# Performance work log

Measured on AMD Instinct MI355X. Metric: run time of the kernel, lower is better.

## Reference

```python
import jax, jax.numpy as jnp
import numpy as np
import math
from jax import lax

NUM_POS = 128        # random_choice in pos_neg_sampling
NUM_TOT = 256        # pos + (128 + negative_padding) always totals 256
POS_W = 10.0         # positive_weight in compute_loss


def _conv(x, w, b, pad):
    y = lax.conv_general_dilated(x, w, (1, 1), pad,
                                 dimension_numbers=('NCHW', 'OIHW', 'NCHW'))
    return y + b[None, :, None, None]


def make_anchor_box(img_h, img_w, gh, gw):
    # torch.range(0, W, W/(gw-1)) == inclusive linspace with gw points
    xs = jnp.linspace(0.0, float(img_w), gw)
    ys = jnp.linspace(0.0, float(img_h), gh)
    gx, gy = jnp.meshgrid(xs, ys, indexing='ij')          # (gw, gh) like torch.meshgrid
    xy = jnp.stack([gx.reshape(-1), gy.reshape(-1)], -1).reshape(gh, gw, 2)
    whs = []
    for area in (128 * 128, 256 * 256, 512 * 512):
        for wr, hr in ((1, 1), (2, 1), (1, 2)):
            u = math.sqrt(area / (wr * hr))
            whs.append((wr * u, hr * u))
    wh = jnp.asarray(whs, jnp.float32)                    # (9, 2)
    xy9 = jnp.broadcast_to(xy[:, :, None, :], (gh, gw, 9, 2))
    wh9 = jnp.broadcast_to(wh[None, None], (gh, gw, 9, 2))
    boxes = jnp.concatenate([xy9, xy9 + wh9], -1)         # x1,y1,x2,y2
    return boxes.reshape(-1, 4)


def pairwise_iou(t, a):
    # t: [T,4], a: [A,4], xyxy -> [T,A]
    lt = jnp.maximum(t[:, None, :2], a[None, :, :2])
    rb = jnp.minimum(t[:, None, 2:], a[None, :, 2:])
    wh = jnp.clip(rb - lt, 0.0)
    inter = wh[..., 0] * wh[..., 1]
    at = (t[:, 2] - t[:, 0]) * (t[:, 3] - t[:, 1])
    aa = (a[:, 2] - a[:, 0]) * (a[:, 3] - a[:, 1])
    return inter / (at[:, None] + aa[None, :] - inter)


def box_encode(anchor, bbox):
    awh = anchor[:, 2:] - anchor[:, :2]
    bwh = bbox[:, 2:] - bbox[:, :2]
    ac = anchor[:, :2] + awh / 2
    bc = bbox[:, :2] + bwh / 2
    dxy = (bc - ac) / awh
    dwh = jnp.log(bwh / awh)
    return jnp.concatenate([dxy, dwh], 1)


def rpn_forward(x, target, conv_w, conv_b, bbox_w, bbox_b, score_w, score_b,
                img_h, img_w):
    gh, gw = x.shape[-2], x.shape[-1]
    h = jax.nn.relu(_conv(x[None], conv_w, conv_b, 'SAME'))
    bbox = jax.nn.relu(_conv(h, bbox_w, bbox_b, 'VALID')).reshape(-1, 4)   # [A,4]
    score = jax.nn.relu(_conv(h, score_w, score_b, 'VALID')).reshape(-1, 2)  # [A,2]
    anchors = make_anchor_box(img_h, img_w, gh, gw)                        # [A,4]

    iou = pairwise_iou(target, anchors)                                    # [T,A]
    max_iou = iou.max(0)
    tgt_idx = jnp.argmax(iou, 0)

    # deterministic replacement for np.random.choice sampling (fixed shapes)
    pos_score = jnp.where(max_iou > 0.7, max_iou, -1.0)
    pos_vals, pos_idx = lax.top_k(pos_score, NUM_POS)
    pos_valid = pos_vals > 0.0
    n_pos = jnp.sum(pos_valid.astype(jnp.int32))

    neg_score = jnp.where(max_iou < 0.3, 1.0 - max_iou, -1.0)
    neg_vals, neg_idx = lax.top_k(neg_score, NUM_TOT)
    neg_valid = (neg_vals > 0.0) & (jnp.arange(NUM_TOT) < (NUM_TOT - n_pos))

    bbox_pred = bbox[pos_idx]                                              # [128,4]
    scores_sel = score[jnp.concatenate([pos_idx, neg_idx])]                # [384,2]
    valid = jnp.concatenate([pos_valid, neg_valid]).astype(jnp.float32)

    tgt_scores = jnp.concatenate([
        jnp.tile(jnp.asarray([[1.0, 0.0]], jnp.float32), (NUM_POS, 1)),
        jnp.tile(jnp.asarray([[0.0, 1.0]], jnp.float32), (NUM_TOT, 1))], 0)

    matched = target[tgt_idx[pos_idx]]
    treg = box_encode(anchors[pos_idx], matched)

    ce = -jnp.sum(tgt_scores * jax.nn.log_softmax(scores_sel, -1), -1)
    score_loss = jnp.sum(ce * valid) / jnp.maximum(jnp.sum(valid), 1.0)

    d = bbox_pred - treg
    sl1 = jnp.where(jnp.abs(d) < 1.0, 0.5 * d * d, jnp.abs(d) - 0.5)
    pm = pos_valid.astype(jnp.float32)[:, None]
    reg_loss = jnp.sum(sl1 * pm) / jnp.maximum(jnp.sum(pm) * 4.0, 1.0)

    return score_loss + POS_W * reg_loss


def setup_inputs():
    key = jax.random.key(0)
    ks = jax.random.split(key, 8)
    cin, gh, gw, nt = 512, 128, 128, 64
    x = jax.random.normal(ks[0], (cin, gh, gw), jnp.float32)
    cxy = jax.random.uniform(ks[1], (nt, 2), minval=300.0, maxval=1748.0)
    wh = jax.random.uniform(ks[2], (nt, 2), minval=64.0, maxval=512.0)
    target = jnp.concatenate([cxy - wh / 2, cxy + wh / 2], -1)
    conv_w = jax.random.normal(ks[3], (cin, cin, 3, 3), jnp.float32) * 0.02
    conv_b = jnp.zeros((cin,), jnp.float32)
    bbox_w = jax.random.normal(ks[4], (36, cin, 1, 1), jnp.float32) * 0.02
    bbox_b = jnp.zeros((36,), jnp.float32)
    score_w = jax.random.normal(ks[5], (18, cin, 1, 1), jnp.float32) * 0.02
    score_b = jnp.zeros((18,), jnp.float32)
    return {'x': x, 'target': target, 'conv_w': conv_w, 'conv_b': conv_b,
            'bbox_w': bbox_w, 'bbox_b': bbox_b, 'score_w': score_w,
            'score_b': score_b, 'img_h': 2048, 'img_w': 2048}


def reference(x, target, conv_w, conv_b, bbox_w, bbox_b, score_w, score_b,
              img_h, img_w):
    return rpn_forward(x, target, conv_w, conv_b, bbox_w, bbox_b,
                       score_w, score_b, img_h, img_w)
```

## Files before the change

kernel.cpp:

```cpp
#include <hip/hip_runtime.h>
#include <cstdint>
#include <cstddef>

typedef unsigned long long ull;
typedef __bf16 bf16x8 __attribute__((ext_vector_type(8)));
typedef float f32x4 __attribute__((ext_vector_type(4)));

#define NA     147456
#define NT     64
#define KDIM   4608
#define NTASK  1280
#define CAND_CAP 4096
#define KSPLIT 4
#define NIOUB  576
#define NTRB   2048
#define NPREP2 512
#define NIMCB  2880

#define OFF_WB2   0
#define OFF_P2    4718592
#define OFF_H4    16515072
#define OFF_XT    27000832
#define OFF_MIOU  43778048
#define OFF_CAND  44367872
#define OFF_CPB   45547520
#define OFF_CBZ   45549824
#define OFF_NPOS  45552128
#define OFF_POSA  45552132
#define OFF_TREG  45552648
#define OFF_TASKS 45554696
#define OFF_OUT   45559816

#define UANC 90.509667991878f
__device__ __constant__ float WKa[9] = {128.0f, 2.0f*UANC, UANC, 256.0f, 4.0f*UANC, 2.0f*UANC, 512.0f, 8.0f*UANC, 4.0f*UANC};
__device__ __constant__ float HKa[9] = {128.0f, UANC, 2.0f*UANC, 256.0f, 2.0f*UANC, 4.0f*UANC, 512.0f, 4.0f*UANC, 8.0f*UANC};

__device__ __forceinline__ float iou_one(float x1, float y1, float x2, float y2, float4 t) {
#pragma clang fp contract(off)
  float ltx = fmaxf(t.x, x1), lty = fmaxf(t.y, y1);
  float rbx = fminf(t.z, x2), rby = fminf(t.w, y2);
  float wx = fmaxf(rbx - ltx, 0.0f);
  float wy = fmaxf(rby - lty, 0.0f);
  float inter = wx * wy;
  float at = (t.z - t.x) * (t.w - t.y);
  float aa = (x2 - x1) * (y2 - y1);
  return inter / ((at + aa) - inter);
}

__device__ __forceinline__ unsigned short f2bf(float f) {
  unsigned int u = __float_as_uint(f);
  unsigned int r = (u + 0x7fffu + ((u >> 16) & 1u)) >> 16;
  return (unsigned short)r;
}

__global__ __launch_bounds__(256) void k_pi(const float* __restrict__ cw,
    unsigned short* __restrict__ Wb2, const float* __restrict__ x,
    unsigned short* __restrict__ xtb,
    const float* __restrict__ tgt, const int* __restrict__ imw,
    const int* __restrict__ imh, float* __restrict__ miou,
    ull* __restrict__ cand, int* __restrict__ cpb, int* __restrict__ cbz) {
  __shared__ __align__(16) char smem[20480];
  int blk = blockIdx.x;
  int tid = threadIdx.x;
  if (blk >= NIOUB + NTRB) {
    float* row = (float*)smem;
    int m = blk - (NIOUB + NTRB);
    const float* src = cw + (size_t)m * KDIM;
    for (int f = tid; f < KDIM; f += 256) {
      int cin = f / 9;
      row[cin * 10 + (f - cin * 9)] = src[f];
    }
    __syncthreads();
    for (int kc = tid; kc < 576; kc += 256) {
      int r = kc >> 6, c8 = kc & 63;
      int base = c8 * 80 + r;
      unsigned short o[8];
      #pragma unroll
      for (int j = 0; j < 8; ++j) o[j] = f2bf(row[base + j * 10]);
      *(uint4*)(Wb2 + ((size_t)kc * 512 + m) * 8) = *(const uint4*)o;
    }
    return;
  }
  if (blk >= NIOUB) {
    float* tile = (float*)smem;
    int tb = blk - NIOUB;
    int pix0 = (tb & 255) * 64;
    int cin0 = (tb >> 8) * 64;
    int pr = tid & 15, cr = tid >> 4;
    #pragma unroll
    for (int i = 0; i < 4; ++i) {
      int cin = cr + i * 16;
      float4 v = *(const float4*)(x + (size_t)(cin0 + cin) * 16384 + pix0 + pr * 4);
      tile[cin * 65 + pr * 4 + 0] = v.x;
      tile[cin * 65 + pr * 4 + 1] = v.y;
      tile[cin * 65 + pr * 4 + 2] = v.z;
      tile[cin * 65 + pr * 4 + 3] = v.w;
    }
    __syncthreads();
    #pragma unroll
    for (int i = 0; i < 4; ++i) {
      int pix = cr + i * 16;
      unsigned short o[4] = {f2bf(tile[(pr * 4 + 0) * 65 + pix]),
                             f2bf(tile[(pr * 4 + 1) * 65 + pix]),
                             f2bf(tile[(pr * 4 + 2) * 65 + pix]),
                             f2bf(tile[(pr * 4 + 3) * 65 + pix])};
      *(uint2*)(xtb + (size_t)(pix0 + pix) * 512 + cin0 + pr * 4) = *(const uint2*)o;
    }
    return;
  }
  float4* ts = (float4*)smem;
  int* wz = (int*)(smem + 1024);
  int* wc = wz + 4;
  if (tid < NT) ts[tid] = ((const float4*)tgt)[tid];
  __syncthreads();
  int a = blk * 256 + tid;
  int k = a % 9;
  int pq = a / 9;
  int p = pq >> 7, q = pq & 127;
  float dx = (float)(*imw) / 127.0f;
  float dyl = (float)(*imh) / 127.0f;
  float x1 = (float)p * dx, y1 = (float)q * dyl;
  float x2 = x1 + WKa[k], y2 = y1 + HKa[k];
  float best = -1.0f;
  #pragma unroll 8
  for (int t = 0; t < NT; ++t) best = fmaxf(best, iou_one(x1, y1, x2, y2, ts[t]));
  miou[a] = best;
  int lane = tid & 63, w = tid >> 6;
  ull bz = __ballot(best == 0.0f);
  bool isc = best > 0.7f;
  ull bc = __ballot(isc);
  if (lane == 0) { wz[w] = (int)__popcll(bz); wc[w] = (int)__popcll(bc); }
  __syncthreads();
  if (tid == 0) {
    cbz[blk] = wz[0] + wz[1] + wz[2] + wz[3];
    cpb[blk] = wc[0] + wc[1] + wc[2] + wc[3];
  }
  if (isc) {
    int woff = 0;
    for (int i = 0; i < w; ++i) woff += wc[i];
    int rank = woff + (int)__popcll(bc & ((1ull << lane) - 1ull));
    cand[blk * 256 + rank] = ((ull)__float_as_uint(best) << 32) | (ull)(0xFFFFFFFFu - (unsigned)a);
  }
}

__global__ __launch_bounds__(256) void k_selA(const ull* __restrict__ cand,
    const int* __restrict__ cpb, int* __restrict__ nposp, int* __restrict__ posa) {
  __shared__ ull keys[CAND_CAP];
  __shared__ ull bnd[1024];
  __shared__ int hist[1024];
  __shared__ int cpbL[576];
  __shared__ int base576[577];
  __shared__ int wtot[4];
  __shared__ int selCnt, bndCnt, Tbin, mAbove;
  int tid = threadIdx.x;
  int lane = tid & 63;
  for (int i = tid; i < 576; i += 256) cpbL[i] = cpb[i];
  for (int i = tid; i < 1024; i += 256) hist[i] = 0;
  __syncthreads();
  int e0 = 0, e1 = 0, sA = 0, scanA = 0;
  if (tid < 192) {
    e0 = cpbL[3 * tid]; e1 = cpbL[3 * tid + 1]; int e2 = cpbL[3 * tid + 2];
    sA = e0 + e1 + e2;
    scanA = sA;
    for (int off = 1; off < 64; off <<= 1) {
      int v = __shfl_up(scanA, off);
      if (lane >= off) scanA += v;
    }
    if (lane == 63) wtot[tid >> 6] = scanA;
  }
  __syncthreads();
  if (tid < 192) {
    int w = tid >> 6;
    int woff = 0;
    for (int i = 0; i < w; ++i) woff += wtot[i];
    int excl = woff + scanA - sA;
    base576[3 * tid]     = excl;
    base576[3 * tid + 1] = excl + e0;
    base576[3 * tid + 2] = excl + e0 + e1;
    if (tid == 191) base576[576] = excl + sA;
  }
  __syncthreads();
  int cnt = base576[576]; if (cnt > CAND_CAP) cnt = CAND_CAP;
  for (int i = tid; i < CAND_CAP; i += 256) if (i >= cnt) keys[i] = 0ull;
  for (int rk = tid; rk < cnt; rk += 256) {
    int lo = 0, hi = 576;
    while (hi - lo > 1) { int mid = (lo + hi) >> 1; if (base576[mid] <= rk) lo = mid; else hi = mid; }
    keys[rk] = cand[lo * 256 + (rk - base576[lo])];
  }
  __syncthreads();
  if (cnt <= 128) {
    if (tid < cnt) posa[tid] = (int)(0xFFFFFFFFu - (unsigned)(keys[tid] & 0xFFFFFFFFull));
    if (tid == 0) *nposp = cnt;
    return;
  }
  for (int i = tid; i < cnt; i += 256) {
    unsigned ib = (unsigned)(keys[i] >> 32);
    atomicAdd(&hist[(ib - 0x3F333334u) >> 13], 1);
  }
  __syncthreads();
  if (tid < 64) {
    int s = 0;
    #pragma unroll
    for (int t = 0; t < 16; ++t) s += hist[tid * 16 + t];
    int S = s;
    #pragma unroll
    for (int off = 1; off < 64; off <<= 1) {
      int u = __shfl_down(S, off);
      if (tid + off < 64) S += u;
    }
    ull mask = __ballot(S >= 128);
    int g = 63 - __clzll(mask);
    int aboveS = __shfl(S, (g + 1 < 64) ? g + 1 : 63);
    if (g == 63) aboveS = 0;
    if (tid == 0) {
      int run = aboveS, T = g * 16 + 15;
      for (int b = g * 16 + 15; b >= g * 16; --b) {
        int h = hist[b];
        if (run + h >= 128) { T = b; break; }
        run += h;
      }
      Tbin = T; mAbove = run; selCnt = 0; bndCnt = 0;
    }
  }
  __syncthreads();
  int T = Tbin, m = mAbove;
  for (int i = tid; i < cnt; i += 256) {
    ull kk = keys[i];
    unsigned ib = (unsigned)(kk >> 32);
    int b = (int)((ib - 0x3F333334u) >> 13);
    if (b > T) {
      int r = atomicAdd(&selCnt, 1);
      posa[r] = (int)(0xFFFFFFFFu - (unsigned)(kk & 0xFFFFFFFFull));
    } else if (b == T) {
      int r = atomicAdd(&bndCnt, 1);
      if (r < 1024) bnd[r] = kk;
    }
  }
  __syncthreads();
  int B = bndCnt;
  int need = 128 - m;
  if (B <= 1024) {
    int n2 = 2; while (n2 < B) n2 <<= 1;
    for (int i = tid; i < n2; i += 256) if (i >= B) bnd[i] = 0ull;
    for (int size = 2; size <= n2; size <<= 1)
      for (int stride = size >> 1; stride > 0; stride >>= 1) {
        __syncthreads();
        for (int t = tid; t < n2 / 2; t += 256) {
          int i = 2 * t - (t & (stride - 1));
          int j = i + stride;
          ull a = bnd[i], b2 = bnd[j];
          bool desc = ((i & size) == 0);
          if (desc ? (a < b2) : (a > b2)) { bnd[i] = b2; bnd[j] = a; }
        }
      }
    __syncthreads();
    if (tid < need) posa[m + tid] = (int)(0xFFFFFFFFu - (unsigned)(bnd[tid] & 0xFFFFFFFFull));
  } else {
    for (int size = 2; size <= CAND_CAP; size <<= 1)
      for (int stride = size >> 1; stride > 0; stride >>= 1) {
        __syncthreads();
        for (int t = tid; t < CAND_CAP / 2; t += 256) {
          int i = 2 * t - (t & (stride - 1));
          int j = i + stride;
          ull a = keys[i], b2 = keys[j];
          bool desc = ((i & size) == 0);
          if (desc ? (a < b2) : (a > b2)) { keys[i] = b2; keys[j] = a; }
        }
      }
    __syncthreads();
    if (tid < 128) posa[tid] = (int)(0xFFFFFFFFu - (unsigned)(keys[tid] & 0xFFFFFFFFull));
  }
  if (tid == 0) *nposp = 128;
}

__global__ __launch_bounds__(256) void k_selB(const float* __restrict__ miou,
    const int* __restrict__ cbz, const float* __restrict__ tgt,
    const int* __restrict__ imw, const int* __restrict__ imh,
    const int* __restrict__ nposp, const int* __restrict__ posa,
    float* __restrict__ treg, int* __restrict__ tasks) {
  __shared__ int nzbase[145];
  __shared__ float4 ts[NT];
  __shared__ int posi[128];
  __shared__ int negA[256];
  __shared__ int wsum[4];
  int tid = threadIdx.x;
  int lane = tid & 63;
  if (tid < NT) ts[tid] = ((const float4*)tgt)[tid];
  int np = *nposp;
  if (tid < np) posi[tid] = posa[tid];
  int sB = 0, scanB = 0;
  if (tid < 144) {
    int4 cz4 = *(const int4*)(cbz + 4 * tid);
    sB = cz4.x + cz4.y + cz4.z + cz4.w;
    scanB = sB;
    for (int off = 1; off < 64; off <<= 1) {
      int v = __shfl_up(scanB, off);
      if (lane >= off) scanB += v;
    }
    bool last = (tid < 128) ? (lane == 63) : (tid == 143);
    if (last) wsum[tid >> 6] = scanB;
  }
  __syncthreads();
  if (tid < 144) {
    int w = tid >> 6;
    int woff = 0;
    for (int i = 0; i < w; ++i) woff += wsum[i];
    nzbase[tid] = woff + scanB - sB;
    if (tid == 143) nzbase[144] = woff + scanB;
  }
  __syncthreads();
  int w = tid >> 6;
  for (int j = 0; j < 144; ++j) {
    if (nzbase[j] >= 256) break;
    int a0 = j * 1024 + tid * 4;
    float4 m4 = *(const float4*)(miou + a0);
    int f0 = (m4.x == 0.0f), f1 = (m4.y == 0.0f), f2 = (m4.z == 0.0f), f3 = (m4.w == 0.0f);
    int tsum = f0 + f1 + f2 + f3;
    int scan = tsum;
    for (int off = 1; off < 64; off <<= 1) {
      int v = __shfl_up(scan, off);
      if (lane >= off) scan += v;
    }
    if (lane == 63) wsum[w] = scan;
    __syncthreads();
    int woff = nzbase[j];
    for (int i = 0; i < w; ++i) woff += wsum[i];
    int r = woff + scan - tsum;
    if (f0) { if (r < 256) negA[r] = a0;     r++; }
    if (f1) { if (r < 256) negA[r] = a0 + 1; r++; }
    if (f2) { if (r < 256) negA[r] = a0 + 2; r++; }
    if (f3) { if (r < 256) negA[r] = a0 + 3;      }
    __syncthreads();
  }
  __syncthreads();
  if (tid < np) {
    int a = posi[tid];
    int k = a % 9; int pq = a / 9; int p = pq >> 7, q = pq & 127;
    float dx = (float)(*imw) / 127.0f, dyl = (float)(*imh) / 127.0f;
    float x1 = (float)p * dx, y1 = (float)q * dyl;
    float x2 = x1 + WKa[k], y2 = y1 + HKa[k];
    float best = -1.0f; int bt = 0;
    for (int t = 0; t < NT; ++t) {
      float v = iou_one(x1, y1, x2, y2, ts[t]);
      if (v > best) { best = v; bt = t; }
    }
    float4 m = ts[bt];
    float aw = x2 - x1, ah = y2 - y1;
    float acx = x1 + aw * 0.5f, acy = y1 + ah * 0.5f;
    float bwd = m.z - m.x, bhd = m.w - m.y;
    float bcx = m.x + bwd * 0.5f, bcy = m.y + bhd * 0.5f;
    treg[tid * 4 + 0] = (bcx - acx) / aw;
    treg[tid * 4 + 1] = (bcy - acy) / ah;
    treg[tid * 4 + 2] = logf(bwd / aw);
    treg[tid * 4 + 3] = logf(bhd / ah);
  }
  for (int t = tid; t < NTASK; t += 256) {
    int rec = 0;
    if (t < 768) {
      int s = t / 6, jj = t - s * 6;
      if (s < np) {
        int a = posi[s];
        int f, wr, xx;
        if (jj < 4) { f = 4 * a; wr = f >> 14; xx = (f & 127) + jj; }
        else        { f = 2 * a; wr = 36 + (f >> 14); xx = (f & 127) + (jj - 4); }
        int yy = (f >> 7) & 127;
        rec = (int)(0x80000000u | ((unsigned)wr << 16) | ((unsigned)yy << 8) | (unsigned)xx);
      }
    } else {
      int s = (t - 768) >> 1, jj = (t - 768) & 1;
      if (s < 256 - np) {
        int a = negA[s];
        int f = 2 * a; int wr = 36 + (f >> 14); int yy = (f >> 7) & 127; int xx = (f & 127) + jj;
        rec = (int)(0x80000000u | ((unsigned)wr << 16) | ((unsigned)yy << 8) | (unsigned)xx);
      }
    }
    tasks[t] = rec;
  }
}

__global__ __launch_bounds__(256) void k_im2col(const unsigned short* __restrict__ xtb,
    const int* __restrict__ tasks, unsigned short* __restrict__ P2) {
  int idx = blockIdx.x * 256 + threadIdx.x;
  int t = idx / 576;
  int kc = idx - t * 576;
  int r = kc >> 6, c8 = kc & 63;
  int rec = tasks[t];
  uint4 frag = {0u, 0u, 0u, 0u};
  if (rec < 0) {
    int py = (rec >> 8) & 127, px = rec & 127;
    int dy = r / 3;
    int yy = py + dy - 1, xx = px + (r - dy * 3) - 1;
    if (yy >= 0 && yy < 128 && xx >= 0 && xx < 128)
      frag = *(const uint4*)(xtb + (size_t)(yy * 128 + xx) * 512 + c8 * 8);
  }
  *(uint4*)(P2 + ((size_t)kc * NTASK + t) * 8) = frag;
}

__global__ __launch_bounds__(256) void k_mfma(const unsigned short* __restrict__ Wb2,
    const unsigned short* __restrict__ P2, const int* __restrict__ nposp,
    float* __restrict__ H4) {
  int npos = *nposp;
  int tt0 = blockIdx.x * 128;
  int posend = 6 * npos, negend = 768 + 2 * (256 - npos);
  if (!((tt0 < posend) || ((tt0 + 128 > 768) && (tt0 < negend)))) return;
  int c0 = blockIdx.y * 128;
  int ks = blockIdx.z;
  int tid = threadIdx.x;
  int wave = tid >> 6, lane = tid & 63;
  int quad = lane >> 4, r = lane & 15;
  int m_base = c0 + (wave & 1) * 64;
  int n_base = tt0 + (wave >> 1) * 64;
  int kc0 = ks * 144 + quad;
  const bf16x8* Ab = (const bf16x8*)Wb2 + ((size_t)kc0 * 512 + m_base + r);
  const bf16x8* Bb = (const bf16x8*)P2 + ((size_t)kc0 * NTASK + n_base + r);

  f32x4 acc[4][4];
  #pragma unroll
  for (int i = 0; i < 4; ++i)
    #pragma unroll
    for (int j = 0; j < 4; ++j) acc[i][j] = (f32x4){0.f, 0.f, 0.f, 0.f};

  bf16x8 a[4], b[4];
  #pragma unroll
  for (int mi = 0; mi < 4; ++mi) a[mi] = Ab[mi * 16];
  #pragma unroll
  for (int ni = 0; ni < 4; ++ni) b[ni] = Bb[ni * 16];

  for (int s = 0; s < 36; ++s) {
    bf16x8 an[4], bn[4];
    if (s < 35) {
      const bf16x8* An = Ab + (size_t)(s + 1) * 4 * 512;
      const bf16x8* Bn = Bb + (size_t)(s + 1) * 4 * NTASK;
      #pragma unroll
      for (int mi = 0; mi < 4; ++mi) an[mi] = An[mi * 16];
      #pragma unroll
      for (int ni = 0; ni < 4; ++ni) bn[ni] = Bn[ni * 16];
    }
    #pragma unroll
    for (int mi = 0; mi < 4; ++mi)
      #pragma unroll
      for (int ni = 0; ni < 4; ++ni)
        acc[mi][ni] = __builtin_amdgcn_mfma_f32_16x16x32_bf16(a[mi], b[ni], acc[mi][ni], 0, 0, 0);
    if (s < 35) {
      #pragma unroll
      for (int mi = 0; mi < 4; ++mi) a[mi] = an[mi];
      #pragma unroll
      for (int ni = 0; ni < 4; ++ni) b[ni] = bn[ni];
    }
  }
  size_t hb = (size_t)ks * NTASK;
  #pragma unroll
  for (int mi = 0; mi < 4; ++mi) {
    int c = m_base + mi * 16 + quad * 4;
    #pragma unroll
    for (int ni = 0; ni < 4; ++ni) {
      int t = n_base + ni * 16 + r;
      *(f32x4*)(H4 + (hb + t) * 512 + c) = acc[mi][ni];
    }
  }
}

__global__ __launch_bounds__(256) void k_out(const float* __restrict__ H4,
    const int* __restrict__ tasks,
    const float* __restrict__ cb, const float* __restrict__ bw,
    const float* __restrict__ bb, const float* __restrict__ sw,
    const float* __restrict__ sb, float* __restrict__ outv) {
  int wave = threadIdx.x >> 6, lane = threadIdx.x & 63;
  int t = blockIdx.x * 4 + wave;
  int rec = tasks[t];
  if (rec >= 0) return;
  int wr = (rec >> 16) & 63;
  const float* wrow = (wr < 36) ? (bw + wr * 512) : (sw + (wr - 36) * 512);
  float s = 0.0f;
  #pragma unroll
  for (int it = 0; it < 8; ++it) {
    int c = it * 64 + lane;
    size_t o = (size_t)t * 512 + c;
    float hv = H4[o] + H4[o + 1280 * 512] + H4[o + 2 * 1280 * 512] + H4[o + 3 * 1280 * 512] + cb[c];
    s = fmaf(fmaxf(hv, 0.0f), wrow[c], s);
  }
  #pragma unroll
  for (int off = 32; off > 0; off >>= 1) s += __shfl_down(s, off);
  if (lane == 0) {
    float b = (wr < 36) ? bb[wr] : sb[wr - 36];
    outv[t] = fmaxf(s + b, 0.0f);
  }
}

__global__ __launch_bounds__(256) void k_loss(const float* __restrict__ outv,
    const float* __restrict__ treg, const int* __restrict__ nposp,
    float* __restrict__ out) {
  __shared__ float r1[256], r2[256];
  int tid = threadIdx.x;
  int np = *nposp;
  float ce = 0.0f;
  for (int r = tid; r < 384; r += 256) {
    bool valid = (r < 128) ? (r < np) : ((r - 128) < 256 - np);
    if (valid) {
      int t0 = (r < 128) ? (r * 6 + 4) : (768 + 2 * (r - 128));
      float s0 = outv[t0], s1 = outv[t0 + 1];
      float mm = fmaxf(s0, s1);
      float lse = mm + logf(expf(s0 - mm) + expf(s1 - mm));
      ce += lse - ((r < 128) ? s0 : s1);
    }
  }
  float rg = 0.0f;
  for (int r = tid; r < 512; r += 256) {
    if ((r >> 2) < np) {
      float d = outv[(r >> 2) * 6 + (r & 3)] - treg[r];
      float ad = fabsf(d);
      rg += (ad < 1.0f) ? 0.5f * d * d : ad - 0.5f;
    }
  }
  r1[tid] = ce; r2[tid] = rg;
  __syncthreads();
  for (int s = 128; s > 0; s >>= 1) {
    if (tid < s) { r1[tid] += r1[tid + s]; r2[tid] += r2[tid + s]; }
    __syncthreads();
  }
  if (tid == 0) {
    float score_loss = r1[0] / 256.0f;
    float reg_loss = r2[0] / fmaxf(4.0f * (float)np, 1.0f);
    out[0] = score_loss + 10.0f * reg_loss;
  }
}

extern "C" void kernel_launch(void* const* d_in, const int* in_sizes, int n_in,
                              void* d_out, int out_size, void* d_ws, size_t ws_size,
                              hipStream_t stream) {
  const float* x   = (const float*)d_in[0];
  const float* tgt = (const float*)d_in[1];
  const float* cw  = (const float*)d_in[2];
  const float* cb  = (const float*)d_in[3];
  const float* bw  = (const float*)d_in[4];
  const float* bb  = (const float*)d_in[5];
  const float* sw  = (const float*)d_in[6];
  const float* sb  = (const float*)d_in[7];
  const int* imh   = (const int*)d_in[8];
  const int* imw   = (const int*)d_in[9];

  char* ws = (char*)d_ws;
  unsigned short* Wb2 = (unsigned short*)(ws + OFF_WB2);
  unsigned short* P2  = (unsigned short*)(ws + OFF_P2);
  float* H4    = (float*)(ws + OFF_H4);
  unsigned short* xtb = (unsigned short*)(ws + OFF_XT);
  float* miou  = (float*)(ws + OFF_MIOU);
  ull*   cand  = (ull*)(ws + OFF_CAND);
  int*   cpb   = (int*)(ws + OFF_CPB);
  int*   cbz   = (int*)(ws + OFF_CBZ);
  int*   nposp = (int*)(ws + OFF_NPOS);
  int*   posa  = (int*)(ws + OFF_POSA);
  float* treg  = (float*)(ws + OFF_TREG);
  int*   tasks = (int*)(ws + OFF_TASKS);
  float* outv  = (float*)(ws + OFF_OUT);
  float* out   = (float*)d_out;

  k_pi    <<<dim3(NIOUB + NTRB + NPREP2), dim3(256), 0, stream>>>(cw, Wb2, x, xtb, tgt, imw, imh, miou, cand, cpb, cbz);
  k_selA  <<<dim3(1),             dim3(256), 0, stream>>>(cand, cpb, nposp, posa);
  k_selB  <<<dim3(1),             dim3(256), 0, stream>>>(miou, cbz, tgt, imw, imh, nposp, posa, treg, tasks);
  k_im2col<<<dim3(NIMCB),         dim3(256), 0, stream>>>(xtb, tasks, P2);
  k_mfma  <<<dim3(10, 4, KSPLIT), dim3(256), 0, stream>>>(Wb2, P2, nposp, H4);
  k_out   <<<dim3(320),           dim3(256), 0, stream>>>(H4, tasks, cb, bw, bb, sw, sb, outv);
  k_loss  <<<dim3(1),             dim3(256), 0, stream>>>(outv, treg, nposp, out);
}
```

Baseline: 164.9 us.

## Use implicit im2col via padded NHWC input and merge selection kernels

The transposed bf16 input is now written into a zero-padded 130x130 layout, and a small zero region is set up for tasks that are not positive or negative. The GEMM kernel gathers its 3x3 patch operands directly from that layout, so the separate im2col kernel and its patch buffer go away. The two single-block selection kernels are merged into one, which removes a launch and a global round trip of the positive indices. The cost is scattered B-operand loads in the MFMA loop, which are less coalesced than the old packed patch buffer.

```diff
diff --git a/kernel.cpp b/kernel.cpp
--- a/kernel.cpp
+++ b/kernel.cpp
@@ -15,21 +15,20 @@
 #define NIOUB  576
 #define NTRB   2048
 #define NPREP2 512
-#define NIMCB  2880
+#define NZERO  197
 
 #define OFF_WB2   0
-#define OFF_P2    4718592
-#define OFF_H4    16515072
-#define OFF_XT    27000832
-#define OFF_MIOU  43778048
-#define OFF_CAND  44367872
-#define OFF_CPB   45547520
-#define OFF_CBZ   45549824
-#define OFF_NPOS  45552128
-#define OFF_POSA  45552132
-#define OFF_TREG  45552648
-#define OFF_TASKS 45554696
-#define OFF_OUT   45559816
+#define OFF_XT    4718592
+#define OFF_ZERO  22024192
+#define OFF_H4    22302720
+#define OFF_MIOU  32788480
+#define OFF_CAND  33378304
+#define OFF_CPB   34557952
+#define OFF_CBZ   34560256
+#define OFF_NPOS  34562560
+#define OFF_TREG  34562576
+#define OFF_TASKS 34564624
+#define OFF_OUT   34569744
 
 #define UANC 90.509667991878f
 __device__ __constant__ float WKa[9] = {128.0f, 2.0f*UANC, UANC, 256.0f, 4.0f*UANC, 2.0f*UANC, 512.0f, 8.0f*UANC, 4.0f*UANC};
@@ -53,15 +52,37 @@
   return (unsigned short)r;
 }
 
+__device__ __forceinline__ int boff(int kcb) {
+  int rk = kcb >> 6;
+  int dy = (rk * 11) >> 5;
+  int dxo = rk - dy * 3;
+  return (dy * 130 + dxo) * 512 + (kcb & 63) * 8;
+}
+
 __global__ __launch_bounds__(256) void k_pi(const float* __restrict__ cw,
     unsigned short* __restrict__ Wb2, const float* __restrict__ x,
-    unsigned short* __restrict__ xtb,
+    unsigned short* __restrict__ xtb, unsigned short* __restrict__ zrg,
     const float* __restrict__ tgt, const int* __restrict__ imw,
     const int* __restrict__ imh, float* __restrict__ miou,
     ull* __restrict__ cand, int* __restrict__ cpb, int* __restrict__ cbz) {
   __shared__ __align__(16) char smem[20480];
   int blk = blockIdx.x;
   int tid = threadIdx.x;
+  if (blk >= NIOUB + NTRB + NPREP2) {
+    int g = (blk - (NIOUB + NTRB + NPREP2)) * 256 + tid;
+    uint4 z = {0u, 0u, 0u, 0u};
+    if (g < 17408) {
+      *(uint4*)(zrg + g * 8) = z;
+    } else {
+      int h = g - 17408;
+      int pixi = h >> 6, j = h & 63;
+      int yy, xx;
+      if (pixi < 260) { yy = (pixi < 130) ? 0 : 129; xx = (pixi < 130) ? pixi : pixi - 130; }
+      else { int p2 = pixi - 260; if (p2 < 128) { yy = 1 + p2; xx = 0; } else { yy = p2 - 127; xx = 129; } }
+      *(uint4*)(xtb + (size_t)(yy * 130 + xx) * 512 + j * 8) = z;
+    }
+    return;
+  }
   if (blk >= NIOUB + NTRB) {
     float* row = (float*)smem;
     int m = blk - (NIOUB + NTRB);
@@ -100,11 +121,13 @@
     #pragma unroll
     for (int i = 0; i < 4; ++i) {
       int pix = cr + i * 16;
+      int plin = pix0 + pix;
+      int py = plin >> 7, px = plin & 127;
       unsigned short o[4] = {f2bf(tile[(pr * 4 + 0) * 65 + pix]),
                              f2bf(tile[(pr * 4 + 1) * 65 + pix]),
                              f2bf(tile[(pr * 4 + 2) * 65 + pix]),
                              f2bf(tile[(pr * 4 + 3) * 65 + pix])};
-      *(uint2*)(xtb + (size_t)(pix0 + pix) * 512 + cin0 + pr * 4) = *(const uint2*)o;
+      *(uint2*)(xtb + (size_t)((py + 1) * 130 + (px + 1)) * 512 + cin0 + pr * 4) = *(const uint2*)o;
     }
     return;
   }
@@ -143,8 +166,11 @@
   }
 }
 
-__global__ __launch_bounds__(256) void k_selA(const ull* __restrict__ cand,
-    const int* __restrict__ cpb, int* __restrict__ nposp, int* __restrict__ posa) {
+__global__ __launch_bounds__(256) void k_sel(const ull* __restrict__ cand,
+    const int* __restrict__ cpb, const float* __restrict__ miou,
+    const int* __restrict__ cbz, const float* __restrict__ tgt,
+    const int* __restrict__ imw, const int* __restrict__ imh,
+    int* __restrict__ nposp, float* __restrict__ treg, int* __restrict__ tasks) {
   __shared__ ull keys[CAND_CAP];
   __shared__ ull bnd[1024];
   __shared__ int hist[1024];
@@ -152,8 +178,15 @@
   __shared__ int base576[577];
   __shared__ int wtot[4];
   __shared__ int selCnt, bndCnt, Tbin, mAbove;
+  __shared__ int posi[128];
+  __shared__ int npS;
+  __shared__ int nzbase[145];
+  __shared__ float4 ts[NT];
+  __shared__ int negA[256];
+  __shared__ int wsum[4];
   int tid = threadIdx.x;
   int lane = tid & 63;
+  if (tid < NT) ts[tid] = ((const float4*)tgt)[tid];
   for (int i = tid; i < 576; i += 256) cpbL[i] = cpb[i];
   for (int i = tid; i < 1024; i += 256) hist[i] = 0;
   __syncthreads();
@@ -189,105 +222,90 @@
   }
   __syncthreads();
   if (cnt <= 128) {
-    if (tid < cnt) posa[tid] = (int)(0xFFFFFFFFu - (unsigned)(keys[tid] & 0xFFFFFFFFull));
-    if (tid == 0) *nposp = cnt;
-    return;
-  }
-  for (int i = tid; i < cnt; i += 256) {
-    unsigned ib = (unsigned)(keys[i] >> 32);
-    atomicAdd(&hist[(ib - 0x3F333334u) >> 13], 1);
-  }
-  __syncthreads();
-  if (tid < 64) {
-    int s = 0;
-    #pragma unroll
-    for (int t = 0; t < 16; ++t) s += hist[tid * 16 + t];
-    int S = s;
-    #pragma unroll
-    for (int off = 1; off < 64; off <<= 1) {
-      int u = __shfl_down(S, off);
-      if (tid + off < 64) S += u;
-    }
-    ull mask = __ballot(S >= 128);
-    int g = 63 - __clzll(mask);
-    int aboveS = __shfl(S, (g + 1 < 64) ? g + 1 : 63);
-    if (g == 63) aboveS = 0;
-    if (tid == 0) {
-      int run = aboveS, T = g * 16 + 15;
-      for (int b = g * 16 + 15; b >= g * 16; --b) {
-        int h = hist[b];
-        if (run + h >= 128) { T = b; break; }
-        run += h;
+    if (tid < cnt) posi[tid] = (int)(0xFFFFFFFFu - (unsigned)(keys[tid] & 0xFFFFFFFFull));
+    if (tid == 0) { npS = cnt; *nposp = cnt; }
+  } else {
+    for (int i = tid; i < cnt; i += 256) {
+      unsigned ib = (unsigned)(keys[i] >> 32);
+      atomicAdd(&hist[(ib - 0x3F333334u) >> 13], 1);
+    }
+    __syncthreads();
+    if (tid < 64) {
+      int s = 0;
+      #pragma unroll
+      for (int t = 0; t < 16; ++t) s += hist[tid * 16 + t];
+      int S = s;
+      #pragma unroll
+      for (int off = 1; off < 64; off <<= 1) {
+        int u = __shfl_down(S, off);
+        if (tid + off < 64) S += u;
       }
-      Tbin = T; mAbove = run; selCnt = 0; bndCnt = 0;
-    }
-  }
-  __syncthreads();
-  int T = Tbin, m = mAbove;
-  for (int i = tid; i < cnt; i += 256) {
-    ull kk = keys[i];
-    unsigned ib = (unsigned)(kk >> 32);
-    int b = (int)((ib - 0x3F333334u) >> 13);
-    if (b > T) {
-      int r = atomicAdd(&selCnt, 1);
-      posa[r] = (int)(0xFFFFFFFFu - (unsigned)(kk & 0xFFFFFFFFull));
-    } else if (b == T) {
-      int r = atomicAdd(&bndCnt, 1);
-      if (r < 1024) bnd[r] = kk;
-    }
-  }
-  __syncthreads();
-  int B = bndCnt;
-  int need = 128 - m;
-  if (B <= 1024) {
-    int n2 = 2; while (n2 < B) n2 <<= 1;
-    for (int i = tid; i < n2; i += 256) if (i >= B) bnd[i] = 0ull;
-    for (int size = 2; size <= n2; size <<= 1)
-      for (int stride = size >> 1; stride > 0; stride >>= 1) {
-        __syncthreads();
-        for (int t = tid; t < n2 / 2; t += 256) {
-          int i = 2 * t - (t & (stride - 1));
-          int j = i + stride;
-          ull a = bnd[i], b2 = bnd[j];
-          bool desc = ((i & size) == 0);
-          if (desc ? (a < b2) : (a > b2)) { bnd[i] = b2; bnd[j] = a; }
+      ull mask = __ballot(S >= 128);
+      int g = 63 - __clzll(mask);
+      int aboveS = __shfl(S, (g + 1 < 64) ? g + 1 : 63);
+      if (g == 63) aboveS = 0;
+      if (tid == 0) {
+        int run = aboveS, T = g * 16 + 15;
+        for (int b = g * 16 + 15; b >= g * 16; --b) {
+          int h = hist[b];
+          if (run + h >= 128) { T = b; break; }
+          run += h;
         }
+        Tbin = T; mAbove = run; selCnt = 0; bndCnt = 0;
       }
-    __syncthreads();
-    if (tid < need) posa[m + tid] = (int)(0xFFFFFFFFu - (unsigned)(bnd[tid] & 0xFFFFFFFFull));
-  } else {
-    for (int size = 2; size <= CAND_CAP; size <<= 1)
-      for (int stride = size >> 1; stride > 0; stride >>= 1) {
-        __syncthreads();
-        for (int t = tid; t < CAND_CAP / 2; t += 256) {
-          int i = 2 * t - (t & (stride - 1));
-          int j = i + stride;
-          ull a = keys[i], b2 = keys[j];
-          bool desc = ((i & size) == 0);
-          if (desc ? (a < b2) : (a > b2)) { keys[i] = b2; keys[j] = a; }
+    }
+    __syncthreads();
+    int T = Tbin, m = mAbove;
+    for (int i = tid; i < cnt; i += 256) {
+      ull kk = keys[i];
+      unsigned ib = (unsigned)(kk >> 32);
+      int b = (int)((ib - 0x3F333334u) >> 13);
+      if (b > T) {
+        int r = atomicAdd(&selCnt, 1);
+        posi[r] = (int)(0xFFFFFFFFu - (unsigned)(kk & 0xFFFFFFFFull));
+      } else if (b == T) {
+        int r = atomicAdd(&bndCnt, 1);
+        if (r < 1024) bnd[r] = kk;
+      }
+    }
+    __syncthreads();
+    int B = bndCnt;
+    int need = 128 - m;
+    if (B <= 1024) {
+      int n2 = 2; while (n2 < B) n2 <<= 1;
+      for (int i = tid; i < n2; i += 256) if (i >= B) bnd[i] = 0ull;
+      for (int size = 2; size <= n2; size <<= 1)
+        for (int stride = size >> 1; stride > 0; stride >>= 1) {
+          __syncthreads();
+          for (int t = tid; t < n2 / 2; t += 256) {
+            int i = 2 * t - (t & (stride - 1));
+            int j = i + stride;
+            ull a = bnd[i], b2 = bnd[j];
+            bool desc = ((i & size) == 0);
+            if (desc ? (a < b2) : (a > b2)) { bnd[i] = b2; bnd[j] = a; }
+          }
         }
-      }
-    __syncthreads();
-    if (tid < 128) posa[tid] = (int)(0xFFFFFFFFu - (unsigned)(keys[tid] & 0xFFFFFFFFull));
-  }
-  if (tid == 0) *nposp = 128;
-}
-
-__global__ __launch_bounds__(256) void k_selB(const float* __restrict__ miou,
-    const int* __restrict__ cbz, const float* __restrict__ tgt,
-    const int* __restrict__ imw, const int* __restrict__ imh,
-    const int* __restrict__ nposp, const int* __restrict__ posa,
-    float* __restrict__ treg, int* __restrict__ tasks) {
-  __shared__ int nzbase[145];
-  __shared__ float4 ts[NT];
-  __shared__ int posi[128];
-  __shared__ int negA[256];
-  __shared__ int wsum[4];
-  int tid = threadIdx.x;
-  int lane = tid & 63;
-  if (tid < NT) ts[tid] = ((const float4*)tgt)[tid];
-  int np = *nposp;
-  if (tid < np) posi[tid] = posa[tid];
+      __syncthreads();
+      if (tid < need) posi[m + tid] = (int)(0xFFFFFFFFu - (unsigned)(bnd[tid] & 0xFFFFFFFFull));
+    } else {
+      for (int size = 2; size <= CAND_CAP; size <<= 1)
+        for (int stride = size >> 1; stride > 0; stride >>= 1) {
+          __syncthreads();
+          for (int t = tid; t < CAND_CAP / 2; t += 256) {
+            int i = 2 * t - (t & (stride - 1));
+            int j = i + stride;
+            ull a = keys[i], b2 = keys[j];
+            bool desc = ((i & size) == 0);
+            if (desc ? (a < b2) : (a > b2)) { keys[i] = b2; keys[j] = a; }
+          }
+        }
+      __syncthreads();
+      if (tid < 128) posi[tid] = (int)(0xFFFFFFFFu - (unsigned)(keys[tid] & 0xFFFFFFFFull));
+    }
+    if (tid == 0) { npS = 128; *nposp = 128; }
+  }
+  __syncthreads();
+  int np = npS;
   int sB = 0, scanB = 0;
   if (tid < 144) {
     int4 cz4 = *(const int4*)(cbz + 4 * tid);
@@ -378,26 +396,9 @@
   }
 }
 
-__global__ __launch_bounds__(256) void k_im2col(const unsigned short* __restrict__ xtb,
-    const int* __restrict__ tasks, unsigned short* __restrict__ P2) {
-  int idx = blockIdx.x * 256 + threadIdx.x;
-  int t = idx / 576;
-  int kc = idx - t * 576;
-  int r = kc >> 6, c8 = kc & 63;
-  int rec = tasks[t];
-  uint4 frag = {0u, 0u, 0u, 0u};
-  if (rec < 0) {
-    int py = (rec >> 8) & 127, px = rec & 127;
-    int dy = r / 3;
-    int yy = py + dy - 1, xx = px + (r - dy * 3) - 1;
-    if (yy >= 0 && yy < 128 && xx >= 0 && xx < 128)
-      frag = *(const uint4*)(xtb + (size_t)(yy * 128 + xx) * 512 + c8 * 8);
-  }
-  *(uint4*)(P2 + ((size_t)kc * NTASK + t) * 8) = frag;
-}
-
 __global__ __launch_bounds__(256) void k_mfma(const unsigned short* __restrict__ Wb2,
-    const unsigned short* __restrict__ P2, const int* __restrict__ nposp,
+    const unsigned short* __restrict__ xtb, const unsigned short* __restrict__ zrg,
+    const int* __restrict__ tasks, const int* __restrict__ nposp,
     float* __restrict__ H4) {
   int npos = *nposp;
   int tt0 = blockIdx.x * 128;
@@ -412,7 +413,16 @@
   int n_base = tt0 + (wave >> 1) * 64;
   int kc0 = ks * 144 + quad;
   const bf16x8* Ab = (const bf16x8*)Wb2 + ((size_t)kc0 * 512 + m_base + r);
-  const bf16x8* Bb = (const bf16x8*)P2 + ((size_t)kc0 * NTASK + n_base + r);
+
+  const unsigned short* Bp[4];
+  #pragma unroll
+  for (int ni = 0; ni < 4; ++ni) {
+    int rec = tasks[n_base + ni * 16 + r];
+    int pix = (rec < 0) ? (((rec >> 8) & 127) * 130 + (rec & 127)) : 0;
+    const unsigned short* base = (rec < 0) ? xtb : zrg;
+    Bp[ni] = base + (size_t)pix * 512 + quad * 8;
+  }
+  int kcb = ks * 144;
 
   f32x4 acc[4][4];
   #pragma unroll
@@ -423,18 +433,19 @@
   bf16x8 a[4], b[4];
   #pragma unroll
   for (int mi = 0; mi < 4; ++mi) a[mi] = Ab[mi * 16];
-  #pragma unroll
-  for (int ni = 0; ni < 4; ++ni) b[ni] = Bb[ni * 16];
+  int ob0 = boff(kcb);
+  #pragma unroll
+  for (int ni = 0; ni < 4; ++ni) b[ni] = *(const bf16x8*)(Bp[ni] + ob0);
 
   for (int s = 0; s < 36; ++s) {
     bf16x8 an[4], bn[4];
     if (s < 35) {
       const bf16x8* An = Ab + (size_t)(s + 1) * 4 * 512;
-      const bf16x8* Bn = Bb + (size_t)(s + 1) * 4 * NTASK;
+      int ob = boff(kcb + 4 * (s + 1));
       #pragma unroll
       for (int mi = 0; mi < 4; ++mi) an[mi] = An[mi * 16];
       #pragma unroll
-      for (int ni = 0; ni < 4; ++ni) bn[ni] = Bn[ni * 16];
+      for (int ni = 0; ni < 4; ++ni) bn[ni] = *(const bf16x8*)(Bp[ni] + ob);
     }
     #pragma unroll
     for (int mi = 0; mi < 4; ++mi)
@@ -541,25 +552,22 @@
 
   char* ws = (char*)d_ws;
   unsigned short* Wb2 = (unsigned short*)(ws + OFF_WB2);
-  unsigned short* P2  = (unsigned short*)(ws + OFF_P2);
+  unsigned short* xtb = (unsigned short*)(ws + OFF_XT);
+  unsigned short* zrg = (unsigned short*)(ws + OFF_ZERO);
   float* H4    = (float*)(ws + OFF_H4);
-  unsigned short* xtb = (unsigned short*)(ws + OFF_XT);
   float* miou  = (float*)(ws + OFF_MIOU);
   ull*   cand  = (ull*)(ws + OFF_CAND);
   int*   cpb   = (int*)(ws + OFF_CPB);
   int*   cbz   = (int*)(ws + OFF_CBZ);
   int*   nposp = (int*)(ws + OFF_NPOS);
-  int*   posa  = (int*)(ws + OFF_POSA);
   float* treg  = (float*)(ws + OFF_TREG);
   int*   tasks = (int*)(ws + OFF_TASKS);
   float* outv  = (float*)(ws + OFF_OUT);
   float* out   = (float*)d_out;
 
-  k_pi    <<<dim3(NIOUB + NTRB + NPREP2), dim3(256), 0, stream>>>(cw, Wb2, x, xtb, tgt, imw, imh, miou, cand, cpb, cbz);
-  k_selA  <<<dim3(1),             dim3(256), 0, stream>>>(cand, cpb, nposp, posa);
-  k_selB  <<<dim3(1),             dim3(256), 0, stream>>>(miou, cbz, tgt, imw, imh, nposp, posa, treg, tasks);
-  k_im2col<<<dim3(NIMCB),         dim3(256), 0, stream>>>(xtb, tasks, P2);
-  k_mfma  <<<dim3(10, 4, KSPLIT), dim3(256), 0, stream>>>(Wb2, P2, nposp, H4);
-  k_out   <<<dim3(320),           dim3(256), 0, stream>>>(H4, tasks, cb, bw, bb, sw, sb, outv);
-  k_loss  <<<dim3(1),             dim3(256), 0, stream>>>(outv, treg, nposp, out);
-}
+  k_pi   <<<dim3(NIOUB + NTRB + NPREP2 + NZERO), dim3(256), 0, stream>>>(cw, Wb2, x, xtb, zrg, tgt, imw, imh, miou, cand, cpb, cbz);
+  k_sel  <<<dim3(1),              dim3(256), 0, stream>>>(cand, cpb, miou, cbz, tgt, imw, imh, nposp, treg, tasks);
+  k_mfma <<<dim3(10, 4, KSPLIT),  dim3(256), 0, stream>>>(Wb2, xtb, zrg, tasks, nposp, H4);
+  k_out  <<<dim3(320),            dim3(256), 0, stream>>>(H4, tasks, cb, bw, bb, sw, sb, outv);
+  k_loss <<<dim3(1),              dim3(256), 0, stream>>>(outv, treg, nposp, out);
+}
```

After: 156.0 us. 1.06x faster.
